# Optimization experiments

Measured on AMD Instinct MI355X. Metric: run time of the kernel, lower is better.

The kernel has to match this reference:

```python
import jax, jax.numpy as jnp
import numpy as np

B, IN_UNITS, IN_CHANNELS, NUM_UNITS, UNIT_SIZE = 256, 8, 1152, 10, 16
NUM_ITERS = 3


def setup_inputs() -> dict:
    key = jax.random.key(0)
    k1, k2 = jax.random.split(key)
    x = jax.random.normal(k1, (B, IN_UNITS, IN_CHANNELS), dtype=jnp.float32)
    # W from nn.Parameter(torch.randn(1, in_channels, num_units, unit_size, in_units)); drop leading 1
    W = jax.random.normal(k2, (IN_CHANNELS, NUM_UNITS, UNIT_SIZE, IN_UNITS), dtype=jnp.float32)
    return {"x": x, "W": W}


def reference(x, W):
    # x: [B, in_units=i, in_channels=j]; original transposes to [B, j, i]
    # u_hat = W @ x : [B, j, n, u]
    batch = x.shape[0]
    u_hat = jnp.einsum('jnui,bij->bjnu', W, x)
    b = jnp.zeros((IN_CHANNELS, NUM_UNITS), dtype=x.dtype)  # b_ij [j, n]
    v = None
    for _ in range(NUM_ITERS):
        # legacy F.softmax on 4D [1,j,n,1] -> dim=1 = in_channels axis
        c = jax.nn.softmax(b, axis=0)  # [j, n]
        s = jnp.einsum('jn,bjnu->bnu', c, u_hat)  # s_j: [B, n, u]
        # squash over dim=2 of [B,1,n,u,1] == num_units axis (axis=1 here)
        mag_sq = jnp.sum(s * s, axis=1, keepdims=True)  # [B, 1, u]
        v = (mag_sq / (1.0 + mag_sq)) * (s / jnp.sqrt(mag_sq))  # [B, n, u]
        # agreement: mean over batch of <u_hat, v>
        b = b + jnp.einsum('bjnu,bnu->jn', u_hat, v) / batch
    return v[..., None]  # [B, num_units, unit_size, 1] == v_j.squeeze(1)
```

## Files before the change

### kernel.cpp

```cpp
#include <hip/hip_runtime.h>
#include <stdint.h>

#define B   256
#define IU  8
#define JC  1152
#define NN  10
#define UU  16
#define NU  160
#define JN  11520
#define WROW 1280
#define NP  9216

typedef short bf16x8 __attribute__((ext_vector_type(8)));
typedef float f32x4  __attribute__((ext_vector_type(4)));

__device__ __forceinline__ short f2bf(float f) {
    union { float f; uint32_t u; } cv; cv.f = f;
    uint32_t u = cv.u;
    uint32_t r = u + 0x7fffu + ((u >> 16) & 1u);
    return (short)(r >> 16);
}
__device__ __forceinline__ float bf2f(short h) {
    union { uint32_t u; float f; } cv; cv.u = ((uint32_t)(unsigned short)h) << 16;
    return cv.f;
}
__device__ __forceinline__ uint32_t bfbits(float f) {
    union { float f; uint32_t u; } cv; cv.f = f;
    return (cv.u + 0x7fffu + ((cv.u >> 16) & 1u)) >> 16;
}
__device__ __forceinline__ uint32_t pk2(float a, float b) {
    return bfbits(a) | (bfbits(b) << 16);
}

__global__ void k_softmax_upd(float* __restrict__ blog, const float* __restrict__ db,
                              float* __restrict__ c) {
    int n = blockIdx.x;
    int tid = threadIdx.x;
    float myv[5]; int cnt = 0;
    for (int j = tid; j < JC; j += 256) {
        float val = blog[j*NN + n] + db[j*NN + n] * (1.f / (float)B);
        blog[j*NN + n] = val;
        myv[cnt++] = val;
    }
    __shared__ float red[256];
    float m = -1e30f;
    for (int k = 0; k < cnt; ++k) m = fmaxf(m, myv[k]);
    red[tid] = m; __syncthreads();
    for (int s = 128; s > 0; s >>= 1) {
        if (tid < s) red[tid] = fmaxf(red[tid], red[tid+s]);
        __syncthreads();
    }
    m = red[0]; __syncthreads();
    float sum = 0.f;
    for (int k = 0; k < cnt; ++k) sum += __expf(myv[k] - m);
    red[tid] = sum; __syncthreads();
    for (int s = 128; s > 0; s >>= 1) {
        if (tid < s) red[tid] += red[tid+s];
        __syncthreads();
    }
    float inv = 1.f / red[0];
    cnt = 0;
    for (int j = tid; j < JC; j += 256)
        c[j*NN + n] = __expf(myv[cnt++] - m) * inv;
}

__global__ void __launch_bounds__(256, 2)
k_gemm1(const float* __restrict__ xg, const float* __restrict__ wg,
        const float* __restrict__ cptr, float* __restrict__ s_part,
        int nchunks) {
    const int kb = blockIdx.x, mt = blockIdx.y;
    const int tid = threadIdx.x;
    const int wv = tid >> 6, lane = tid & 63;
    const int q = lane >> 4, l16 = lane & 15;
    const int b0 = mt * 32;
    const int jb0 = kb * (nchunks * 8);
    const int mfrag = wv >> 1;
    const int ntb = (wv & 1) * 5;

    __shared__ __align__(16) short As[8 * 32 * 8];
    __shared__ __align__(16) short Bs[8 * 160 * 8];

    f32x4 acc[5];
    #pragma unroll
    for (int nt = 0; nt < 5; ++nt) acc[nt] = (f32x4){0.f, 0.f, 0.f, 0.f};

    for (int jc = 0; jc < nchunks; ++jc) {
        const int j0 = jb0 + jc * 8;
        __syncthreads();
        #pragma unroll
        for (int p = 0; p < 2; ++p) {
            int idx = tid + 256 * p;
            int jq  = idx & 1;
            int row = idx >> 1;
            int bl = row >> 3, ii = row & 7;
            const float4 xv = *reinterpret_cast<const float4*>(
                &xg[(size_t)(b0 + bl) * NP + ii * JC + j0 + jq*4]);
            int jjb = jq * 4;
            As[((jjb+0)*32 + bl)*8 + ii] = f2bf(xv.x);
            As[((jjb+1)*32 + bl)*8 + ii] = f2bf(xv.y);
            As[((jjb+2)*32 + bl)*8 + ii] = f2bf(xv.z);
            As[((jjb+3)*32 + bl)*8 + ii] = f2bf(xv.w);
        }
        #pragma unroll
        for (int p = 0; p < 5; ++p) {
            int ridx = tid + 256 * p;
            int jj = ridx / 160;
            int nu = ridx - jj * 160;
            int j  = j0 + jj;
            const float4* wp = reinterpret_cast<const float4*>(
                &wg[(size_t)j * WROW + (size_t)nu * 8]);
            float4 f0 = wp[0], f1 = wp[1];
            float cc = cptr ? cptr[j * NN + (nu >> 4)] : (1.0f / (float)JC);
            uint4 d;
            d.x = pk2(f0.x * cc, f0.y * cc);
            d.y = pk2(f0.z * cc, f0.w * cc);
            d.z = pk2(f1.x * cc, f1.y * cc);
            d.w = pk2(f1.z * cc, f1.w * cc);
            *reinterpret_cast<uint4*>(&Bs[(size_t)ridx * 8]) = d;
        }
        __syncthreads();
        #pragma unroll
        for (int s = 0; s < 2; ++s) {
            int jj = s*4 + q;
            bf16x8 av = *reinterpret_cast<const bf16x8*>(
                &As[((jj*32 + mfrag*16 + l16) << 3)]);
            #pragma unroll
            for (int nt = 0; nt < 5; ++nt) {
                bf16x8 bv = *reinterpret_cast<const bf16x8*>(
                    &Bs[((jj*160 + (ntb + nt)*16 + l16) << 3)]);
                acc[nt] = __builtin_amdgcn_mfma_f32_16x16x32_bf16(av, bv, acc[nt], 0, 0, 0);
            }
        }
    }
    float* dst = s_part + (size_t)(kb*8 + mt) * 5120;
    #pragma unroll
    for (int nt = 0; nt < 5; ++nt)
        #pragma unroll
        for (int reg = 0; reg < 4; ++reg)
            dst[(mfrag*16 + q*4 + reg) * 160 + (ntb + nt)*16 + l16] = acc[nt][reg];
}

__global__ void __launch_bounds__(256, 4)
k_red1(const float* __restrict__ s_part, float* __restrict__ partial, int KB) {
    const int o  = blockIdx.x * 256 + threadIdx.x;
    const int kq = blockIdx.y;
    const int kper = KB >> 3;
    const int k0 = kq * kper;
    float s = 0.f;
    for (int r = 0; r < kper; ++r)
        s += s_part[(size_t)(k0 + r) * 40960 + o];
    partial[(size_t)kq * 40960 + o] = s;
}

__global__ void k_reduce_s(const float* __restrict__ partial, float* __restrict__ vdst) {
    const int b = blockIdx.x, t = threadIdx.x;
    const int mt = b >> 5, bl = b & 31;
    const size_t o = (size_t)mt * 5120 + bl * 160 + t;
    float s = 0.f;
    #pragma unroll
    for (int kq = 0; kq < 8; ++kq)
        s += partial[(size_t)kq * 40960 + o];

    __shared__ float sv[NU];
    __shared__ float fb[UU];
    sv[t] = s; __syncthreads();
    if (t < UU) {
        float m = 0.f;
        #pragma unroll
        for (int n = 0; n < NN; ++n) { float z = sv[n*16 + t]; m = fmaf(z, z, m); }
        fb[t] = sqrtf(m) / (1.f + m);
    }
    __syncthreads();
    vdst[(size_t)b * NU + t] = s * fb[t & 15];
}

__global__ void __launch_bounds__(256, 2)
k_vxg(const float* __restrict__ vg, const float* __restrict__ xg,
      float* __restrict__ G) {
    const int np0 = blockIdx.x * 64, m0 = blockIdx.y * 32;
    const int tid = threadIdx.x;
    const int wv = tid >> 6, lane = tid & 63;
    const int q = lane >> 4, l16 = lane & 15;

    __shared__ __align__(16) short Ash[8 * 32 * 8];
    __shared__ __align__(16) short Asl[8 * 32 * 8];
    __shared__ __align__(16) short Bsh[8 * 64 * 8];
    __shared__ __align__(16) short Bsl[8 * 64 * 8];

    f32x4 acc[2];
    acc[0] = (f32x4){0.f,0.f,0.f,0.f};
    acc[1] = (f32x4){0.f,0.f,0.f,0.f};

    for (int ks = 0; ks < 4; ++ks) {
        const int b0 = ks * 64;
        __syncthreads();
        #pragma unroll
        for (int p = 0; p < 8; ++p) {
            int idx = tid + 256 * p;
            int bb = idx >> 5, ml = idx & 31;
            float vv = vg[(size_t)(b0 + bb) * NU + m0 + ml];
            short hi = f2bf(vv);
            short lo = f2bf(vv - bf2f(hi));
            int a = ((bb >> 3) * 32 + ml) * 8 + (bb & 7);
            Ash[a] = hi; Asl[a] = lo;
        }
        #pragma unroll
        for (int p = 0; p < 16; ++p) {
            int idx = tid + 256 * p;
            int bb = idx >> 6, nl = idx & 63;
            float xv = xg[(size_t)(b0 + bb) * NP + np0 + nl];
            short hi = f2bf(xv);
            short lo = f2bf(xv - bf2f(hi));
            int a = ((bb >> 3) * 64 + nl) * 8 + (bb & 7);
            Bsh[a] = hi; Bsl[a] = lo;
        }
        __syncthreads();
        #pragma unroll
        for (int s = 0; s < 2; ++s) {
            int kc = s*4 + q;
            bf16x8 bh = *reinterpret_cast<const bf16x8*>(&Bsh[((kc*64 + wv*16 + l16) << 3)]);
            bf16x8 bl = *reinterpret_cast<const bf16x8*>(&Bsl[((kc*64 + wv*16 + l16) << 3)]);
            #pragma unroll
            for (int mt = 0; mt < 2; ++mt) {
                bf16x8 ah = *reinterpret_cast<const bf16x8*>(&Ash[((kc*32 + mt*16 + l16) << 3)]);
                bf16x8 al = *reinterpret_cast<const bf16x8*>(&Asl[((kc*32 + mt*16 + l16) << 3)]);
                acc[mt] = __builtin_amdgcn_mfma_f32_16x16x32_bf16(ah, bh, acc[mt], 0, 0, 0);
                acc[mt] = __builtin_amdgcn_mfma_f32_16x16x32_bf16(ah, bl, acc[mt], 0, 0, 0);
                acc[mt] = __builtin_amdgcn_mfma_f32_16x16x32_bf16(al, bh, acc[mt], 0, 0, 0);
            }
        }
    }
    #pragma unroll
    for (int mt = 0; mt < 2; ++mt)
        #pragma unroll
        for (int reg = 0; reg < 4; ++reg) {
            int m  = m0 + mt*16 + q*4 + reg;
            G[(size_t)m * NP + np0 + wv*16 + l16] = acc[mt][reg];
        }
}

__global__ void k_wg_db(const float* __restrict__ wg, const float* __restrict__ G,
                        float* __restrict__ db) {
    const int j0 = blockIdx.x * 64, n = blockIdx.y;
    const int tid = threadIdx.x;
    const int jl = tid & 63, up = tid >> 6;
    const int j = j0 + jl;

    const float4* wp = reinterpret_cast<const float4*>(
        wg + (size_t)j * WROW + n * 128 + up * 32);
    float acc = 0.f;
    #pragma unroll
    for (int q4 = 0; q4 < 4; ++q4) {
        int u = up*4 + q4;
        const float* gp = G + (size_t)(n*16 + u) * NP + j;
        float4 w0 = wp[q4*2], w1 = wp[q4*2 + 1];
        acc = fmaf(w0.x, gp[0*JC], acc);
        acc = fmaf(w0.y, gp[1*JC], acc);
        acc = fmaf(w0.z, gp[2*JC], acc);
        acc = fmaf(w0.w, gp[3*JC], acc);
        acc = fmaf(w1.x, gp[4*JC], acc);
        acc = fmaf(w1.y, gp[5*JC], acc);
        acc = fmaf(w1.z, gp[6*JC], acc);
        acc = fmaf(w1.w, gp[7*JC], acc);
    }
    __shared__ float red[4][64];
    red[up][jl] = acc;
    __syncthreads();
    if (tid < 64)
        db[(size_t)(j0 + tid) * NN + n] =
            red[0][tid] + red[1][tid] + red[2][tid] + red[3][tid];
}

extern "C" void kernel_launch(void* const* d_in, const int* in_sizes, int n_in,
                              void* d_out, int out_size, void* d_ws, size_t ws_size,
                              hipStream_t stream) {
    const float* x = (const float*)d_in[0];
    const float* w = (const float*)d_in[1];
    float* out = (float*)d_out;

    float* ws      = (float*)d_ws;
    float* blog    = ws;
    float* c       = blog + JN;
    float* db      = c + JN;
    float* v       = db + JN;
    float* s_part  = v + (size_t)B*NU;
    int KB = 72;
    size_t fixed = 3*(size_t)JN + (size_t)B*NU;
    while (KB > 8 &&
           (fixed + (size_t)KB*40960 + 8*40960 + 1474560) * 4 > ws_size) KB >>= 1;
    int nchunks = 144 / KB;
    float* partial = s_part + (size_t)KB * 40960;
    float* G       = partial + (size_t)8 * 40960;

    hipMemsetAsync(blog, 0, JN * sizeof(float), stream);

    for (int t = 0; t < 3; ++t) {
        k_gemm1<<<dim3(KB, 8), 256, 0, stream>>>(x, w, (t == 0) ? nullptr : c,
                                                 s_part, nchunks);
        k_red1<<<dim3(160, 8), 256, 0, stream>>>(s_part, partial, KB);
        k_reduce_s<<<B, NU, 0, stream>>>(partial, (t == 2) ? out : v);
        if (t < 2) {
            k_vxg<<<dim3(144, 5), 256, 0, stream>>>(v, x, G);
            k_wg_db<<<dim3(18, 10), 256, 0, stream>>>(w, G, db);
            k_softmax_upd<<<NN, 256, 0, stream>>>(blog, db, c);
        }
    }
}
```

Measured before the change: 163.7 us.

## Pre-pack x and c-scaled W to bf16, split gemm1 over all 144 chunks

```diff
diff --git a/kernel.cpp b/kernel.cpp
--- a/kernel.cpp
+++ b/kernel.cpp
@@ -10,6 +10,7 @@
 #define JN  11520
 #define WROW 1280
 #define NP  9216
+#define KB  144
 
 typedef short bf16x8 __attribute__((ext_vector_type(8)));
 typedef float f32x4  __attribute__((ext_vector_type(4)));
@@ -32,104 +33,81 @@
     return bfbits(a) | (bfbits(b) << 16);
 }
 
-__global__ void k_softmax_upd(float* __restrict__ blog, const float* __restrict__ db,
-                              float* __restrict__ c) {
-    int n = blockIdx.x;
-    int tid = threadIdx.x;
-    float myv[5]; int cnt = 0;
-    for (int j = tid; j < JC; j += 256) {
-        float val = blog[j*NN + n] + db[j*NN + n] * (1.f / (float)B);
-        blog[j*NN + n] = val;
-        myv[cnt++] = val;
-    }
-    __shared__ float red[256];
-    float m = -1e30f;
-    for (int k = 0; k < cnt; ++k) m = fmaxf(m, myv[k]);
-    red[tid] = m; __syncthreads();
-    for (int s = 128; s > 0; s >>= 1) {
-        if (tid < s) red[tid] = fmaxf(red[tid], red[tid+s]);
-        __syncthreads();
-    }
-    m = red[0]; __syncthreads();
-    float sum = 0.f;
-    for (int k = 0; k < cnt; ++k) sum += __expf(myv[k] - m);
-    red[tid] = sum; __syncthreads();
-    for (int s = 128; s > 0; s >>= 1) {
-        if (tid < s) red[tid] += red[tid+s];
-        __syncthreads();
-    }
-    float inv = 1.f / red[0];
-    cnt = 0;
-    for (int j = tid; j < JC; j += 256)
-        c[j*NN + n] = __expf(myv[cnt++] - m) * inv;
-}
-
-__global__ void __launch_bounds__(256, 2)
-k_gemm1(const float* __restrict__ xg, const float* __restrict__ wg,
-        const float* __restrict__ cptr, float* __restrict__ s_part,
-        int nchunks) {
+__global__ void k_pack_x(const float* __restrict__ xg, unsigned short* __restrict__ xpk) {
+    const int j0 = blockIdx.x * 32, b0 = blockIdx.y * 32;
+    const int tid = threadIdx.x;
+    __shared__ unsigned short tile[32 * 32 * 8];
+    const int bl = tid >> 3, ii = tid & 7;
+    const float* src = xg + (size_t)(b0 + bl) * NP + ii * JC + j0;
+    #pragma unroll
+    for (int jq = 0; jq < 8; ++jq) {
+        float4 xv = *reinterpret_cast<const float4*>(src + jq * 4);
+        tile[(jq*4+0)*256 + bl*8 + ii] = (unsigned short)bfbits(xv.x);
+        tile[(jq*4+1)*256 + bl*8 + ii] = (unsigned short)bfbits(xv.y);
+        tile[(jq*4+2)*256 + bl*8 + ii] = (unsigned short)bfbits(xv.z);
+        tile[(jq*4+3)*256 + bl*8 + ii] = (unsigned short)bfbits(xv.w);
+    }
+    __syncthreads();
+    const int jj = tid >> 3, g = tid & 7;
+    const uint4* lsrc = reinterpret_cast<const uint4*>(tile + jj * 256);
+    uint4* gdst = reinterpret_cast<uint4*>(xpk + (size_t)(j0 + jj) * 2048 + b0 * 8);
+    #pragma unroll
+    for (int k = 0; k < 4; ++k) gdst[g*4 + k] = lsrc[g*4 + k];
+}
+
+__global__ void k_pack_w(const float* __restrict__ wg, const float* __restrict__ cptr,
+                         unsigned short* __restrict__ wpk) {
+    const int j = blockIdx.x, t = threadIdx.x;
+    float4 f = *reinterpret_cast<const float4*>(wg + (size_t)j * WROW + t * 4);
+    float cc = cptr ? cptr[j * NN + (t >> 5)] : (1.0f / (float)JC);
+    uint2 d;
+    d.x = pk2(f.x * cc, f.y * cc);
+    d.y = pk2(f.z * cc, f.w * cc);
+    *reinterpret_cast<uint2*>(wpk + (size_t)j * WROW + t * 4) = d;
+}
+
+__global__ void __launch_bounds__(256, 4)
+k_gemm1(const unsigned short* __restrict__ xpk, const unsigned short* __restrict__ wpk,
+        float* __restrict__ s_part) {
     const int kb = blockIdx.x, mt = blockIdx.y;
     const int tid = threadIdx.x;
     const int wv = tid >> 6, lane = tid & 63;
     const int q = lane >> 4, l16 = lane & 15;
-    const int b0 = mt * 32;
-    const int jb0 = kb * (nchunks * 8);
+    const int b0 = mt * 32, j0 = kb * 8;
     const int mfrag = wv >> 1;
     const int ntb = (wv & 1) * 5;
 
     __shared__ __align__(16) short As[8 * 32 * 8];
     __shared__ __align__(16) short Bs[8 * 160 * 8];
 
+    {
+        int jj = tid >> 5, r = tid & 31;
+        uint4 vv = *reinterpret_cast<const uint4*>(
+            xpk + (size_t)(j0 + jj) * 2048 + b0 * 8 + r * 8);
+        *reinterpret_cast<uint4*>(As + jj * 256 + r * 8) = vv;
+    }
+    {
+        const uint4* src = reinterpret_cast<const uint4*>(wpk + (size_t)j0 * WROW);
+        uint4* dst = reinterpret_cast<uint4*>(Bs);
+        #pragma unroll
+        for (int p = 0; p < 5; ++p) dst[tid + 256 * p] = src[tid + 256 * p];
+    }
+    __syncthreads();
+
     f32x4 acc[5];
     #pragma unroll
     for (int nt = 0; nt < 5; ++nt) acc[nt] = (f32x4){0.f, 0.f, 0.f, 0.f};
 
-    for (int jc = 0; jc < nchunks; ++jc) {
-        const int j0 = jb0 + jc * 8;
-        __syncthreads();
-        #pragma unroll
-        for (int p = 0; p < 2; ++p) {
-            int idx = tid + 256 * p;
-            int jq  = idx & 1;
-            int row = idx >> 1;
-            int bl = row >> 3, ii = row & 7;
-            const float4 xv = *reinterpret_cast<const float4*>(
-                &xg[(size_t)(b0 + bl) * NP + ii * JC + j0 + jq*4]);
-            int jjb = jq * 4;
-            As[((jjb+0)*32 + bl)*8 + ii] = f2bf(xv.x);
-            As[((jjb+1)*32 + bl)*8 + ii] = f2bf(xv.y);
-            As[((jjb+2)*32 + bl)*8 + ii] = f2bf(xv.z);
-            As[((jjb+3)*32 + bl)*8 + ii] = f2bf(xv.w);
-        }
-        #pragma unroll
-        for (int p = 0; p < 5; ++p) {
-            int ridx = tid + 256 * p;
-            int jj = ridx / 160;
-            int nu = ridx - jj * 160;
-            int j  = j0 + jj;
-            const float4* wp = reinterpret_cast<const float4*>(
-                &wg[(size_t)j * WROW + (size_t)nu * 8]);
-            float4 f0 = wp[0], f1 = wp[1];
-            float cc = cptr ? cptr[j * NN + (nu >> 4)] : (1.0f / (float)JC);
-            uint4 d;
-            d.x = pk2(f0.x * cc, f0.y * cc);
-            d.y = pk2(f0.z * cc, f0.w * cc);
-            d.z = pk2(f1.x * cc, f1.y * cc);
-            d.w = pk2(f1.z * cc, f1.w * cc);
-            *reinterpret_cast<uint4*>(&Bs[(size_t)ridx * 8]) = d;
-        }
-        __syncthreads();
-        #pragma unroll
-        for (int s = 0; s < 2; ++s) {
-            int jj = s*4 + q;
-            bf16x8 av = *reinterpret_cast<const bf16x8*>(
-                &As[((jj*32 + mfrag*16 + l16) << 3)]);
-            #pragma unroll
-            for (int nt = 0; nt < 5; ++nt) {
-                bf16x8 bv = *reinterpret_cast<const bf16x8*>(
-                    &Bs[((jj*160 + (ntb + nt)*16 + l16) << 3)]);
-                acc[nt] = __builtin_amdgcn_mfma_f32_16x16x32_bf16(av, bv, acc[nt], 0, 0, 0);
-            }
+    #pragma unroll
+    for (int s = 0; s < 2; ++s) {
+        int jj = s*4 + q;
+        bf16x8 av = *reinterpret_cast<const bf16x8*>(
+            &As[((jj*32 + mfrag*16 + l16) << 3)]);
+        #pragma unroll
+        for (int nt = 0; nt < 5; ++nt) {
+            bf16x8 bv = *reinterpret_cast<const bf16x8*>(
+                &Bs[((jj*160 + (ntb + nt)*16 + l16) << 3)]);
+            acc[nt] = __builtin_amdgcn_mfma_f32_16x16x32_bf16(av, bv, acc[nt], 0, 0, 0);
         }
     }
     float* dst = s_part + (size_t)(kb*8 + mt) * 5120;
@@ -141,13 +119,12 @@
 }
 
 __global__ void __launch_bounds__(256, 4)
-k_red1(const float* __restrict__ s_part, float* __restrict__ partial, int KB) {
+k_red1(const float* __restrict__ s_part, float* __restrict__ partial) {
     const int o  = blockIdx.x * 256 + threadIdx.x;
     const int kq = blockIdx.y;
-    const int kper = KB >> 3;
-    const int k0 = kq * kper;
+    const int k0 = kq * 18;
     float s = 0.f;
-    for (int r = 0; r < kper; ++r)
+    for (int r = 0; r < 18; ++r)
         s += s_part[(size_t)(k0 + r) * 40960 + o];
     partial[(size_t)kq * 40960 + o] = s;
 }
@@ -221,21 +198,21 @@
             bf16x8 bh = *reinterpret_cast<const bf16x8*>(&Bsh[((kc*64 + wv*16 + l16) << 3)]);
             bf16x8 bl = *reinterpret_cast<const bf16x8*>(&Bsl[((kc*64 + wv*16 + l16) << 3)]);
             #pragma unroll
-            for (int mt = 0; mt < 2; ++mt) {
-                bf16x8 ah = *reinterpret_cast<const bf16x8*>(&Ash[((kc*32 + mt*16 + l16) << 3)]);
-                bf16x8 al = *reinterpret_cast<const bf16x8*>(&Asl[((kc*32 + mt*16 + l16) << 3)]);
-                acc[mt] = __builtin_amdgcn_mfma_f32_16x16x32_bf16(ah, bh, acc[mt], 0, 0, 0);
-                acc[mt] = __builtin_amdgcn_mfma_f32_16x16x32_bf16(ah, bl, acc[mt], 0, 0, 0);
-                acc[mt] = __builtin_amdgcn_mfma_f32_16x16x32_bf16(al, bh, acc[mt], 0, 0, 0);
+            for (int mtl = 0; mtl < 2; ++mtl) {
+                bf16x8 ah = *reinterpret_cast<const bf16x8*>(&Ash[((kc*32 + mtl*16 + l16) << 3)]);
+                bf16x8 al = *reinterpret_cast<const bf16x8*>(&Asl[((kc*32 + mtl*16 + l16) << 3)]);
+                acc[mtl] = __builtin_amdgcn_mfma_f32_16x16x32_bf16(ah, bh, acc[mtl], 0, 0, 0);
+                acc[mtl] = __builtin_amdgcn_mfma_f32_16x16x32_bf16(ah, bl, acc[mtl], 0, 0, 0);
+                acc[mtl] = __builtin_amdgcn_mfma_f32_16x16x32_bf16(al, bh, acc[mtl], 0, 0, 0);
             }
         }
     }
     #pragma unroll
-    for (int mt = 0; mt < 2; ++mt)
+    for (int mtl = 0; mtl < 2; ++mtl)
         #pragma unroll
         for (int reg = 0; reg < 4; ++reg) {
-            int m  = m0 + mt*16 + q*4 + reg;
-            G[(size_t)m * NP + np0 + wv*16 + l16] = acc[mt][reg];
+            int m  = m0 + mtl*16 + q*4 + reg;
+            G[(size_t)m * NP + np0 + wv*16 + l16] = acc[mtl][reg];
         }
 }
 
@@ -271,6 +248,38 @@
             red[0][tid] + red[1][tid] + red[2][tid] + red[3][tid];
 }
 
+__global__ void k_softmax_upd(float* __restrict__ blog, const float* __restrict__ db,
+                              float* __restrict__ c) {
+    int n = blockIdx.x;
+    int tid = threadIdx.x;
+    float myv[5]; int cnt = 0;
+    for (int j = tid; j < JC; j += 256) {
+        float val = blog[j*NN + n] + db[j*NN + n] * (1.f / (float)B);
+        blog[j*NN + n] = val;
+        myv[cnt++] = val;
+    }
+    __shared__ float red[256];
+    float m = -1e30f;
+    for (int k = 0; k < cnt; ++k) m = fmaxf(m, myv[k]);
+    red[tid] = m; __syncthreads();
+    for (int s = 128; s > 0; s >>= 1) {
+        if (tid < s) red[tid] = fmaxf(red[tid], red[tid+s]);
+        __syncthreads();
+    }
+    m = red[0]; __syncthreads();
+    float sum = 0.f;
+    for (int k = 0; k < cnt; ++k) sum += __expf(myv[k] - m);
+    red[tid] = sum; __syncthreads();
+    for (int s = 128; s > 0; s >>= 1) {
+        if (tid < s) red[tid] += red[tid+s];
+        __syncthreads();
+    }
+    float inv = 1.f / red[0];
+    cnt = 0;
+    for (int j = tid; j < JC; j += 256)
+        c[j*NN + n] = __expf(myv[cnt++] - m) * inv;
+}
+
 extern "C" void kernel_launch(void* const* d_in, const int* in_sizes, int n_in,
                               void* d_out, int out_size, void* d_ws, size_t ws_size,
                               hipStream_t stream) {
@@ -284,20 +293,18 @@
     float* db      = c + JN;
     float* v       = db + JN;
     float* s_part  = v + (size_t)B*NU;
-    int KB = 72;
-    size_t fixed = 3*(size_t)JN + (size_t)B*NU;
-    while (KB > 8 &&
-           (fixed + (size_t)KB*40960 + 8*40960 + 1474560) * 4 > ws_size) KB >>= 1;
-    int nchunks = 144 / KB;
     float* partial = s_part + (size_t)KB * 40960;
     float* G       = partial + (size_t)8 * 40960;
+    unsigned short* xpk = (unsigned short*)(G + 1474560);
+    unsigned short* wpk = xpk + (size_t)JC * 2048;
 
     hipMemsetAsync(blog, 0, JN * sizeof(float), stream);
+    k_pack_x<<<dim3(36, 8), 256, 0, stream>>>(x, xpk);
 
     for (int t = 0; t < 3; ++t) {
-        k_gemm1<<<dim3(KB, 8), 256, 0, stream>>>(x, w, (t == 0) ? nullptr : c,
-                                                 s_part, nchunks);
-        k_red1<<<dim3(160, 8), 256, 0, stream>>>(s_part, partial, KB);
+        k_pack_w<<<JC, 320, 0, stream>>>(w, (t == 0) ? nullptr : c, wpk);
+        k_gemm1<<<dim3(KB, 8), 256, 0, stream>>>(xpk, wpk, s_part);
+        k_red1<<<dim3(160, 8), 256, 0, stream>>>(s_part, partial);
         k_reduce_s<<<B, NU, 0, stream>>>(partial, (t == 2) ? out : v);
         if (t < 2) {
             k_vxg<<<dim3(144, 5), 256, 0, stream>>>(v, x, G);
```

After: 169.0 us. +3.2%, slower.
